# Kernel tuning notes

Hardware: AMD Instinct MI355X
Metric: run time of the kernel (lower is better)

Reference implementation:

```python
import jax, jax.numpy as jnp
import numpy as np
import math

B = 128        # batch (= bipartite matching N)
L = 16         # detector layers (MAX_LAYER)
E = 768        # n_embd
D = E // 2     # RFF target_dim
H = 12         # n_head
HD = E // H    # head_size
NL = 6         # n_layer
SEQ = 12       # tokens after concats: 3+3 -> 6 -> +currentLayer -> 12
MAX_LAYER = L
LN_EPS = 1e-3  # keras LayerNormalization default


def setup_inputs() -> dict:
    key = jax.random.key(0)
    ks = jax.random.split(key, 8)
    inp = {}
    inp["X"] = jax.random.normal(ks[0], (B, L, 3), dtype=jnp.float32) * 50.0
    inp["targets"] = jax.random.normal(ks[1], (B, L, 3), dtype=jnp.float32)
    # RandomFourierFeatures params (random per-call in original; fixed here):
    # x: xmin=-160,xmax=160,n=9*1024 ; y: n=12*512 ; dE: xmin=0,xmax=230,n=2300
    specs = [(-160.0, 160.0, 9 * 1024), (-160.0, 160.0, 12 * 512), (0.0, 230.0, 2300)]
    om, ph = [], []
    for i, (xmin, xmax, n) in enumerate(specs):
        k1, k2 = jax.random.split(jax.random.fold_in(ks[2], i))
        omin = 2.0 * math.pi / (xmax - xmin)
        lo, hi = math.log(omin / n), math.log(omin)
        om.append(jnp.exp(jax.random.uniform(k1, (D,), minval=lo, maxval=hi)))
        ph.append(jax.random.uniform(k2, (D,)))  # B ~ U(0,1)*scale, scale=1
    inp["omegas"] = jnp.stack(om).astype(jnp.float32)  # (3, D)
    inp["phases"] = jnp.stack(ph).astype(jnp.float32)  # (3, D)
    # np.random.permutation per layer-step, fixed here
    inp["perms"] = jnp.stack(
        [jax.random.permutation(jax.random.fold_in(ks[3], i), B) for i in range(L - 1)]
    ).astype(jnp.int32)  # (L-1, B)
    # transformer weights (stacked over layers)
    kk = jax.random.split(ks[4], 16)
    s = 0.02
    inp["Wq"] = jax.random.normal(kk[0], (NL, E, H, HD)) * s
    inp["bq"] = jnp.zeros((NL, H, HD))
    inp["Wk"] = jax.random.normal(kk[1], (NL, E, H, HD)) * s
    inp["bk"] = jnp.zeros((NL, H, HD))
    inp["Wv"] = jax.random.normal(kk[2], (NL, E, H, HD)) * s
    inp["bv"] = jnp.zeros((NL, H, HD))
    inp["Wo"] = jax.random.normal(kk[3], (NL, H, HD, E)) * s
    inp["bo"] = jnp.zeros((NL, E))
    inp["ln1g"] = jnp.ones((NL, E)); inp["ln1b"] = jnp.zeros((NL, E))
    inp["ln2g"] = jnp.ones((NL, E)); inp["ln2b"] = jnp.zeros((NL, E))
    inp["W1"] = jax.random.normal(kk[4], (NL, E, 4 * E)) * s
    inp["b1f"] = jnp.zeros((NL, 4 * E))
    inp["W2"] = jax.random.normal(kk[5], (NL, 4 * E, E)) * s
    inp["b2f"] = jnp.zeros((NL, E))
    inp["lnfg"] = jnp.ones((E,)); inp["lnfb"] = jnp.zeros((E,))
    inp["Wout"] = jax.random.normal(kk[6], (SEQ * E, 3)) * s
    inp["bout"] = jnp.zeros((3,))
    return inp


def _ln(x, g, b):
    mu = jnp.mean(x, -1, keepdims=True)
    v = jnp.var(x, -1, keepdims=True)
    return (x - mu) * jax.lax.rsqrt(v + LN_EPS) * g + b


def _greedy_match(cost):
    """Greedy bipartite matching: sort all NxN costs ascending, assign first-come.
    Returns row_to_col_match_vec (N,) int32."""
    N = cost.shape[0]
    order = jnp.argsort(cost.reshape(-1))

    def step(carry, k):
        row, col = carry
        i = k // N
        j = k % N
        ok = (row[i] == -1) & (col[j] == -1)
        row = row.at[i].set(jnp.where(ok, j, row[i]))
        col = col.at[j].set(jnp.where(ok, i, col[j]))
        return (row, col), None

    init = (jnp.full((N,), -1, jnp.int32), jnp.full((N,), -1, jnp.int32))
    (row, _), _ = jax.lax.scan(step, init, order)
    return row


def _forward(X, targets, omegas, phases, perms, Wq, bq, Wk, bk, Wv, bv, Wo, bo,
             ln1g, ln1b, ln2g, ln2b, W1, b1f, W2, b2f, lnfg, lnfb, Wout, bout):
    # RFF: (B,L,3) -> (B,L,3,D)
    XS = jnp.cos(X[..., None] * omegas[None, None, :, :] + phases[None, None, :, :])
    losses = []
    scale = 1.0 / math.sqrt(HD)
    for lidx in range(1, L):
        xc = XS[:, -lidx]        # (B,3,D)
        xp = XS[:, -lidx - 1]    # (B,3,D)
        x = jnp.concatenate([xc, xp], axis=2)            # (B,3,E)
        y = targets[:, -lidx + 1]                        # (B,3)
        y_prev = jnp.broadcast_to(y[:, :, None], (B, 3, E))
        x = jnp.concatenate([x, y_prev], axis=1)         # (B,6,E)
        cur = jnp.full_like(x, float(MAX_LAYER - lidx))
        x = jnp.concatenate([x, cur], axis=1)            # (B,12,E)
        x = x[perms[lidx - 1]]                           # batch permutation
        for l in range(NL):
            h = _ln(x, ln1g[l], ln1b[l])
            q = jnp.einsum('bse,ehd->bshd', h, Wq[l]) + bq[l]
            k = jnp.einsum('bse,ehd->bshd', h, Wk[l]) + bk[l]
            v = jnp.einsum('bse,ehd->bshd', h, Wv[l]) + bv[l]
            att = jax.nn.softmax(jnp.einsum('bqhd,bkhd->bhqk', q, k) * scale, axis=-1)
            o = jnp.einsum('bhqk,bkhd->bqhd', att, v)
            x = x + (jnp.einsum('bqhd,hde->bqe', o, Wo[l]) + bo[l])
            h = _ln(x, ln2g[l], ln2b[l])
            x = x + (jnp.maximum(h @ W1[l] + b1f[l], 0.0) @ W2[l] + b2f[l])
        x = _ln(x, lnfg, lnfb).reshape(B, SEQ * E)
        logits = x @ Wout + bout                         # (B,3)
        tgt = targets[:, -lidx]                          # (B,3)
        cost = jnp.sqrt(jnp.sum((logits[:, None, :] - tgt[None, :, :]) ** 2, axis=-1) + 1e-12)
        m = _greedy_match(jax.lax.stop_gradient(cost))
        lm = logits[m]                                   # gather per original
        losses.append(jnp.mean((lm - tgt) ** 2))
    return jnp.mean(jnp.stack(losses))


def reference(X, targets, omegas, phases, perms, Wq, bq, Wk, bk, Wv, bv, Wo, bo,
              ln1g, ln1b, ln2g, ln2b, W1, b1f, W2, b2f, lnfg, lnfb, Wout, bout):
    return _forward(X, targets, omegas, phases, perms, Wq, bq, Wk, bk, Wv, bv, Wo, bo,
                    ln1g, ln1b, ln2g, ln2b, W1, b1f, W2, b2f, lnfg, lnfb, Wout, bout)
```

## Files before the change

### kernel.cpp

```cpp
#include <hip/hip_runtime.h>
#include <hip/hip_bf16.h>
#include <math.h>

#define B_   128
#define L_   16
#define E_   768
#define D_   384
#define H_   12
#define HD_  64
#define NL_  6
#define SEQ_ 12
#define LN_EPS 0.001f
#define WLS   7077888
#define BQS   2304

typedef __attribute__((ext_vector_type(8))) short bf16x8;
typedef __attribute__((ext_vector_type(4))) float f32x4;
typedef unsigned long long u64;

#define GLOAD_LDS16(g, l) \
    __builtin_amdgcn_global_load_lds((__attribute__((address_space(1))) const void*)(g), \
                                     (__attribute__((address_space(3))) void*)(l), 16, 0, 0)

__global__ __launch_bounds__(256) void k_x0(const float* __restrict__ X,
                                            const float* __restrict__ targets,
                                            const int* __restrict__ perms,
                                            const float* __restrict__ om,
                                            const float* __restrict__ ph,
                                            float* __restrict__ x, int cb, int ntok) {
    int i = blockIdx.x * 256 + threadIdx.x;
    if (i >= ntok*E_) return;
    int e   = i % E_;
    int tok = i / E_;
    int s   = tok % SEQ_;
    int bi  = (tok / SEQ_) % B_;
    int c   = tok / (SEQ_*B_);
    int cl  = cb + c;
    int lidx = cl + 1;
    int pb  = perms[cl*B_ + bi];
    float val;
    if (s < 3) {
        int t  = (e < D_) ? (L_ - lidx) : (L_ - lidx - 1);
        int dd = (e < D_) ? e : (e - D_);
        float xv = X[(pb*L_ + t)*3 + s];
        val = cosf(xv * om[s*D_ + dd] + ph[s*D_ + dd]);
    } else if (s < 6) {
        int t = (17 - lidx) & 15;
        val = targets[(pb*L_ + t)*3 + (s - 3)];
    } else {
        val = (float)(L_ - lidx);
    }
    x[i] = val;
}

__global__ __launch_bounds__(256) void k_ln(const float* __restrict__ x,
                                            const float* __restrict__ g,
                                            const float* __restrict__ b,
                                            __hip_bfloat16* __restrict__ h) {
    int gi = blockIdx.x * 256 + threadIdx.x;
    int tok = gi >> 6, lane = gi & 63;
    const float4* xr = (const float4*)(x + (size_t)tok * E_);
    float4 v0 = xr[lane], v1 = xr[lane + 64], v2 = xr[lane + 128];
    float s = v0.x+v0.y+v0.z+v0.w + v1.x+v1.y+v1.z+v1.w + v2.x+v2.y+v2.z+v2.w;
    #pragma unroll
    for (int o = 32; o > 0; o >>= 1) s += __shfl_xor(s, o, 64);
    float mu = s * (1.0f / E_);
    v0.x-=mu; v0.y-=mu; v0.z-=mu; v0.w-=mu;
    v1.x-=mu; v1.y-=mu; v1.z-=mu; v1.w-=mu;
    v2.x-=mu; v2.y-=mu; v2.z-=mu; v2.w-=mu;
    float q = v0.x*v0.x+v0.y*v0.y+v0.z*v0.z+v0.w*v0.w
            + v1.x*v1.x+v1.y*v1.y+v1.z*v1.z+v1.w*v1.w
            + v2.x*v2.x+v2.y*v2.y+v2.z*v2.z+v2.w*v2.w;
    #pragma unroll
    for (int o = 32; o > 0; o >>= 1) q += __shfl_xor(q, o, 64);
    float rstd = rsqrtf(q * (1.0f / E_) + LN_EPS);
    const float4* g4 = (const float4*)g;
    const float4* b4 = (const float4*)b;
    ushort4* h4 = (ushort4*)(h + (size_t)tok * E_);
    #pragma unroll
    for (int k = 0; k < 3; k++) {
        float4 v = (k == 0) ? v0 : (k == 1) ? v1 : v2;
        float4 gg = g4[lane + k*64], bb = b4[lane + k*64];
        ushort4 o;
        o.x = __bfloat16_as_ushort(__float2bfloat16(v.x * rstd * gg.x + bb.x));
        o.y = __bfloat16_as_ushort(__float2bfloat16(v.y * rstd * gg.y + bb.y));
        o.z = __bfloat16_as_ushort(__float2bfloat16(v.z * rstd * gg.z + bb.z));
        o.w = __bfloat16_as_ushort(__float2bfloat16(v.w * rstd * gg.w + bb.w));
        h4[lane + k*64] = o;
    }
}

__global__ __launch_bounds__(256) void k_cvt(const float* __restrict__ Wq,
                                             const float* __restrict__ Wk,
                                             const float* __restrict__ Wv,
                                             const float* __restrict__ Wo,
                                             const float* __restrict__ W1,
                                             const float* __restrict__ W2,
                                             const float* __restrict__ bq,
                                             const float* __restrict__ bk,
                                             const float* __restrict__ bv,
                                             __hip_bfloat16* __restrict__ wl0,
                                             float* __restrict__ bqkv0, int lbase) {
    int bid = blockIdx.x;
    int l   = lbase + bid / 6913;
    bid %= 6913;
    __hip_bfloat16* wl = wl0 + (size_t)(l - lbase) * WLS;
    float* bqkv = bqkv0 + (l - lbase) * BQS;
    int tid = threadIdx.x;
    if (bid == 6912) {
        for (int i = tid; i < 2304; i += 256) {
            float v = (i < 768) ? bq[l*768 + i] : (i < 1536) ? bk[l*768 + i - 768]
                                                             : bv[l*768 + i - 1536];
            bqkv[i] = v;
        }
        return;
    }
    const float* src; __hip_bfloat16* dst; int K, N, ti, tj;
    if (bid < 1728) {
        int part = bid / 576, idx = bid % 576;
        const float* srcs[3] = {Wq, Wk, Wv};
        src = srcs[part] + (size_t)l*768*768; dst = wl + (size_t)part*768*768;
        K = 768; N = 768; tj = idx % 24; ti = idx / 24;
    } else if (bid < 2304) {
        int idx = bid - 1728;
        src = Wo + (size_t)l*768*768; dst = wl + 1769472;
        K = 768; N = 768; tj = idx % 24; ti = idx / 24;
    } else if (bid < 4608) {
        int idx = bid - 2304;
        src = W1 + (size_t)l*768*3072; dst = wl + 2359296;
        K = 768; N = 3072; tj = idx % 96; ti = idx / 96;
    } else {
        int idx = bid - 4608;
        src = W2 + (size_t)l*3072*768; dst = wl + 4718592;
        K = 3072; N = 768; tj = idx % 24; ti = idx / 24;
    }
    __shared__ float tbuf[32][33];
    int tx = tid & 31, ty = tid >> 5;
    #pragma unroll
    for (int p = 0; p < 4; p++) {
        int k = ti*32 + ty + p*8, n = tj*32 + tx;
        tbuf[ty + p*8][tx] = src[(size_t)k*N + n];
    }
    __syncthreads();
    #pragma unroll
    for (int p = 0; p < 4; p++) {
        int n = tj*32 + ty + p*8, k = ti*32 + tx;
        dst[(size_t)n*K + k] = __float2bfloat16(tbuf[tx][ty + p*8]);
    }
}

#define MFMA_BF16(a, b, c) __builtin_amdgcn_mfma_f32_16x16x32_bf16(a, b, c, 0, 0, 0)

__global__ __launch_bounds__(256) void k_gemm128(const __hip_bfloat16* __restrict__ A,
                                                 const __hip_bfloat16* __restrict__ Bt,
                                                 const float* __restrict__ bias,
                                                 void* __restrict__ Cp,
                                                 int K, int ldb, int ldc, int flags) {
    __shared__ __align__(16) char smem[32768];
    const int tid  = threadIdx.x;
    const int lane = tid & 63;
    const int wid  = tid >> 6;
    const int wr   = wid >> 1;
    const int wc   = wid & 1;

    const int gx   = gridDim.x;
    const int nwg  = gx * gridDim.y;
    const int flat = blockIdx.y * gx + blockIdx.x;
    const int q8   = nwg >> 3, r8 = nwg & 7;
    const int xcd  = flat & 7, off8 = flat >> 3;
    const int swz  = (xcd < r8 ? xcd*(q8+1) : r8*(q8+1) + (xcd-r8)*q8) + off8;
    const int m0   = (swz / gx) * 128;
    const int n0   = (swz % gx) * 128;

    const int fr   = lane & 15, fkg = lane >> 4;
    const int NT   = K >> 5;

    const int srow = tid >> 2;
    const int skc  = 8 * ((tid & 3) ^ (srow & 3) ^ ((srow >> 2) & 3));

    const int rsw  = ((fkg ^ (fr & 3) ^ ((fr >> 2) & 3)) << 4);

    f32x4 acc[4][4] = {};

    auto stage = [&](int kt, int buf) {
        char* base = smem + buf*16384;
        const int kk = kt*32 + skc;
        GLOAD_LDS16(A  + (size_t)(m0 +      srow) * K   + kk, base +         tid*16);
        GLOAD_LDS16(A  + (size_t)(m0 + 64 + srow) * K   + kk, base +  4096 + tid*16);
        GLOAD_LDS16(Bt + (size_t)(n0 +      srow) * ldb + kk, base +  8192 + tid*16);
        GLOAD_LDS16(Bt + (size_t)(n0 + 64 + srow) * ldb + kk, base + 12288 + tid*16);
    };
    auto ldA = [&](int buf, int i) -> bf16x8 {
        int row = wr*64 + i*16 + fr;
        return *(const bf16x8*)(smem + buf*16384 + row*64 + rsw);
    };
    auto ldB = [&](int buf, int j) -> bf16x8 {
        int row = wc*64 + j*16 + fr;
        return *(const bf16x8*)(smem + buf*16384 + 8192 + row*64 + rsw);
    };

    stage(0, 0);
    __syncthreads();

    for (int kt = 0; kt < NT; ++kt) {
        const int cur = kt & 1;
        if (kt + 1 < NT) stage(kt + 1, cur ^ 1);
        bf16x8 b[4], a[4];
        #pragma unroll
        for (int j = 0; j < 4; j++) b[j] = ldB(cur, j);
        #pragma unroll
        for (int i = 0; i < 4; i++) a[i] = ldA(cur, i);
        __builtin_amdgcn_s_setprio(1);
        #pragma unroll
        for (int i = 0; i < 4; i++)
            #pragma unroll
            for (int j = 0; j < 4; j++)
                acc[i][j] = MFMA_BF16(a[i], b[j], acc[i][j]);
        __builtin_amdgcn_s_setprio(0);
        __syncthreads();
    }

    const int colL = lane & 15, rowg = (lane >> 4) * 4;
    #pragma unroll
    for (int i = 0; i < 4; i++) {
        #pragma unroll
        for (int j = 0; j < 4; j++) {
            int col = n0 + wc*64 + j*16 + colL;
            float bv = bias ? bias[col] : 0.0f;
            #pragma unroll
            for (int r = 0; r < 4; r++) {
                int row = m0 + wr*64 + i*16 + rowg + r;
                float v = acc[i][j][r] + bv;
                if (flags & 4) v = fmaxf(v, 0.0f);
                size_t off = (size_t)row * ldc + col;
                if (flags & 1)      ((__hip_bfloat16*)Cp)[off] = __float2bfloat16(v);
                else if (flags & 2) ((float*)Cp)[off] += v;
                else                ((float*)Cp)[off] = v;
            }
        }
    }
}

__global__ __launch_bounds__(256) void k_attn(const __hip_bfloat16* __restrict__ qkv,
                                              __hip_bfloat16* __restrict__ o) {
    __shared__ float qs[SEQ_][HD_], ks[SEQ_][HD_], vs[SEQ_][HD_];
    __shared__ float att[SEQ_][SEQ_];
    int blk = blockIdx.x;
    int hh  = blk % H_;
    int cbb = blk / H_;
    int t = threadIdx.x;
    if (t < 96) {
        int s = t >> 3, c = (t & 7) * 8;
        size_t base = (size_t)(cbb*SEQ_ + s) * 2304 + hh*64 + c;
        bf16x8 q8 = *(const bf16x8*)(qkv + base);
        bf16x8 k8 = *(const bf16x8*)(qkv + base + 768);
        bf16x8 v8 = *(const bf16x8*)(qkv + base + 1536);
        #pragma unroll
        for (int j = 0; j < 8; j++) {
            qs[s][c+j] = __uint_as_float((unsigned)(unsigned short)q8[j] << 16);
            ks[s][c+j] = __uint_as_float((unsigned)(unsigned short)k8[j] << 16);
            vs[s][c+j] = __uint_as_float((unsigned)(unsigned short)v8[j] << 16);
        }
    }
    __syncthreads();
    if (t < SEQ_*SEQ_) {
        int qi = t / SEQ_, kj = t % SEQ_;
        float s = 0.f;
        #pragma unroll
        for (int d = 0; d < HD_; d++) s += qs[qi][d] * ks[kj][d];
        att[qi][kj] = s * 0.125f;
    }
    __syncthreads();
    if (t < SEQ_) {
        float mx = -1e30f;
        #pragma unroll
        for (int j = 0; j < SEQ_; j++) mx = fmaxf(mx, att[t][j]);
        float e[SEQ_]; float sum = 0.f;
        #pragma unroll
        for (int j = 0; j < SEQ_; j++) { e[j] = expf(att[t][j] - mx); sum += e[j]; }
        float inv = 1.f / sum;
        #pragma unroll
        for (int j = 0; j < SEQ_; j++) att[t][j] = e[j] * inv;
    }
    __syncthreads();
    for (int i = t; i < SEQ_*HD_; i += 256) {
        int s = i / HD_, d = i % HD_;
        float acc = 0.f;
        #pragma unroll
        for (int j = 0; j < SEQ_; j++) acc += att[s][j] * vs[j][d];
        o[(size_t)(cbb*SEQ_ + s) * 768 + hh*64 + d] = __float2bfloat16(acc);
    }
}

__global__ __launch_bounds__(256) void k_logits(const __hip_bfloat16* __restrict__ hfin,
                                                const float* __restrict__ Wout,
                                                const float* __restrict__ bout,
                                                float* __restrict__ logits, int cb) {
    __shared__ float red[3][256];
    int blk = blockIdx.x;
    int t = threadIdx.x;
    const __hip_bfloat16* row = hfin + (size_t)blk * SEQ_ * E_;
    float a0 = 0.f, a1 = 0.f, a2 = 0.f;
    for (int e = t; e < SEQ_*E_; e += 256) {
        float x = __bfloat162float(row[e]);
        a0 += x * Wout[e*3 + 0]; a1 += x * Wout[e*3 + 1]; a2 += x * Wout[e*3 + 2];
    }
    red[0][t] = a0; red[1][t] = a1; red[2][t] = a2;
    __syncthreads();
    for (int o = 128; o > 0; o >>= 1) {
        if (t < o) { red[0][t] += red[0][t+o]; red[1][t] += red[1][t+o]; red[2][t] += red[2][t+o]; }
        __syncthreads();
    }
    if (t < 3) logits[((size_t)cb*B_ + blk)*3 + t] = red[t][0] + bout[t];
}

__global__ __launch_bounds__(64) void k_match(const float* __restrict__ logits,
                                              const float* __restrict__ targets,
                                              float* __restrict__ losses) {
    __shared__ float cst[128 * 129];
    __shared__ float tg[128][3];
    __shared__ int mrow[128];
    int cl = blockIdx.x, lane = threadIdx.x;
    int lidx = cl + 1;
    for (int j = lane; j < 128; j += 64) {
        const float* tp = &targets[((size_t)j*L_ + (L_ - lidx)) * 3];
        tg[j][0] = tp[0]; tg[j][1] = tp[1]; tg[j][2] = tp[2];
    }
    __syncthreads();
    u64 kc[2];
    #pragma unroll
    for (int hh = 0; hh < 2; hh++) {
        int r = lane + hh*64;
        const float* lg = &logits[(cl*B_ + r) * 3];
        float l0 = lg[0], l1 = lg[1], l2 = lg[2];
        u64 best = ~0ull;
        for (int c = 0; c < 128; c++) {
            float d0 = l0 - tg[c][0], d1 = l1 - tg[c][1], d2 = l2 - tg[c][2];
            float cc = sqrtf(d0*d0 + d1*d1 + d2*d2 + 1e-12f);
            cst[r*129 + c] = cc;
            u64 key = ((u64)__float_as_uint(cc) << 14) | (unsigned)(r*128 + c);
            best = key < best ? key : best;
        }
        kc[hh] = best;
    }
    __syncthreads();
    u64 dead0 = 0, dead1 = 0;
    int done = 0;
    for (int trip = 0; trip < 16640 && done < 128; trip++) {
        u64 b = kc[0] < kc[1] ? kc[0] : kc[1];
        #pragma unroll
        for (int o = 32; o > 0; o >>= 1) {
            u64 x = __shfl_xor(b, o, 64);
            b = x < b ? x : b;
        }
        unsigned e  = (unsigned)b & 0x3fffu;
        unsigned wi = e >> 7, wj = e & 127;
        bool isDead = (((wj < 64) ? (dead0 >> wj) : (dead1 >> (wj - 64))) & 1ull) != 0;
        if (!isDead) {
            if ((wi & 63u) == (unsigned)lane) {
                mrow[wi] = (int)wj;
                kc[wi >> 6] = ~0ull;
            }
            if (wj < 64) dead0 |= 1ull << wj; else dead1 |= 1ull << (wj - 64);
            done++;
        } else {
            float c0 = cst[wi*129 + lane];
            float c1 = cst[wi*129 + lane + 64];
            bool d0b = ((dead0 >> lane) & 1ull) != 0;
            bool d1b = ((dead1 >> lane) & 1ull) != 0;
            u64 k0 = d0b ? ~0ull : (((u64)__float_as_uint(c0) << 14) | (unsigned)(wi*128 + lane));
            u64 k1 = d1b ? ~0ull : (((u64)__float_as_uint(c1) << 14) | (unsigned)(wi*128 + lane + 64));
            u64 nb = k0 < k1 ? k0 : k1;
            #pragma unroll
            for (int o = 32; o > 0; o >>= 1) {
                u64 x = __shfl_xor(nb, o, 64);
                nb = x < nb ? x : nb;
            }
            if ((wi & 63u) == (unsigned)lane) kc[wi >> 6] = nb;
        }
    }
    __syncthreads();
    float a = 0.f;
    #pragma unroll
    for (int hh = 0; hh < 2; hh++) {
        int r = lane + hh*64;
        const float* lg = &logits[(cl*B_ + mrow[r]) * 3];
        float d0 = lg[0]-tg[r][0], d1 = lg[1]-tg[r][1], d2 = lg[2]-tg[r][2];
        a += d0*d0 + d1*d1 + d2*d2;
    }
    #pragma unroll
    for (int o = 32; o > 0; o >>= 1) a += __shfl_xor(a, o, 64);
    if (lane == 0) losses[cl] = a * (1.0f / (B_*3));
}

__global__ void k_final(const float* __restrict__ losses, float* __restrict__ out) {
    float s = 0.f;
    for (int i = 0; i < 15; i++) s += losses[i];
    out[0] = s * (1.0f / 15.0f);
}

extern "C" void kernel_launch(void* const* d_in, const int* in_sizes, int n_in,
                              void* d_out, int out_size, void* d_ws, size_t ws_size,
                              hipStream_t stream) {
    (void)in_sizes; (void)n_in; (void)out_size;
    const float* X       = (const float*)d_in[0];
    const float* targets = (const float*)d_in[1];
    const float* omegas  = (const float*)d_in[2];
    const float* phases  = (const float*)d_in[3];
    const int*   perms   = (const int*)d_in[4];
    const float* Wq  = (const float*)d_in[5];
    const float* bq  = (const float*)d_in[6];
    const float* Wk  = (const float*)d_in[7];
    const float* bk  = (const float*)d_in[8];
    const float* Wv  = (const float*)d_in[9];
    const float* bv  = (const float*)d_in[10];
    const float* Wo  = (const float*)d_in[11];
    const float* bo  = (const float*)d_in[12];
    const float* ln1g = (const float*)d_in[13];
    const float* ln1b = (const float*)d_in[14];
    const float* ln2g = (const float*)d_in[15];
    const float* ln2b = (const float*)d_in[16];
    const float* W1  = (const float*)d_in[17];
    const float* b1f = (const float*)d_in[18];
    const float* W2  = (const float*)d_in[19];
    const float* b2f = (const float*)d_in[20];
    const float* lnfg = (const float*)d_in[21];
    const float* lnfb = (const float*)d_in[22];
    const float* Wout = (const float*)d_in[23];
    const float* bout = (const float*)d_in[24];

    int CL; bool hoist;
    if (ws_size >= 263000000ull)      { CL = 15; hoist = false; }
    else if (ws_size >= 169000000ull) { CL = 5;  hoist = true;  }
    else                              { CL = 5;  hoist = false; }
    int M = CL * B_ * SEQ_;
    bool perLayerCvt = (CL == 15) || !hoist;

    char* wsb = (char*)d_ws;
    size_t off = 0;
    auto alloc = [&](size_t bytes) {
        char* p = wsb + off;
        off += (bytes + 255) & ~(size_t)255;
        return p;
    };
    float*          x      = (float*)alloc((size_t)M*E_*4);
    __hip_bfloat16* h      = (__hip_bfloat16*)alloc((size_t)M*E_*2);
    __hip_bfloat16* qkvh   = (__hip_bfloat16*)alloc((size_t)M*3072*2);
    __hip_bfloat16* wl     = (__hip_bfloat16*)alloc((hoist ? 6 : 1) * (size_t)WLS*2);
    float*          bqkv   = (float*)alloc((hoist ? 6 : 1) * (size_t)BQS*4);
    float*          logits = (float*)alloc(23040);
    float*          losses = (float*)alloc(64);

    if (hoist)
        k_cvt<<<6*6913, 256, 0, stream>>>(Wq, Wk, Wv, Wo, W1, W2, bq, bk, bv, wl, bqkv, 0);

    dim3 gQKV(2304/128, M/128);
    dim3 gF1 (3072/128, M/128);
    dim3 gN  (768/128,  M/128);
    dim3 gLN (M/4);

    for (int cb = 0; cb < 15; cb += CL) {
        k_x0<<<(M*E_)/256, 256, 0, stream>>>(X, targets, perms, omegas, phases, x, cb, M);
        for (int l = 0; l < NL_; l++) {
            __hip_bfloat16* wlp = hoist ? wl + (size_t)l*WLS : wl;
            float*          bqp = hoist ? bqkv + l*BQS : bqkv;
            if (perLayerCvt)
                k_cvt<<<6913, 256, 0, stream>>>(Wq, Wk, Wv, Wo, W1, W2, bq, bk, bv, wlp, bqp, l);
            k_ln<<<gLN, 256, 0, stream>>>(x, ln1g + l*E_, ln1b + l*E_, h);
            k_gemm128<<<gQKV, 256, 0, stream>>>(h, wlp, bqp, qkvh, 768, 768, 2304, 1);
            k_attn<<<CL*B_*H_, 256, 0, stream>>>(qkvh, h);
            k_gemm128<<<gN, 256, 0, stream>>>(h, wlp + 1769472, bo + l*E_, x,
                                              768, 768, 768, 2);
            k_ln<<<gLN, 256, 0, stream>>>(x, ln2g + l*E_, ln2b + l*E_, h);
            k_gemm128<<<gF1, 256, 0, stream>>>(h, wlp + 2359296, b1f + l*3072, qkvh,
                                               768, 768, 3072, 1|4);
            k_gemm128<<<gN, 256, 0, stream>>>(qkvh, wlp + 4718592, b2f + l*E_, x,
                                              3072, 3072, 768, 2);
        }
        k_ln<<<gLN, 256, 0, stream>>>(x, lnfg, lnfb, h);
        k_logits<<<CL*B_, 256, 0, stream>>>(h, Wout, bout, logits, cb);
    }
    k_match<<<15, 64, 0, stream>>>(logits, targets, losses);
    k_final<<<1, 1, 0, stream>>>(losses, (float*)d_out);
}
```

Before: 4.541 ms.

## Stage GEMM epilogue through LDS for coalesced stores; cheaper wave min reduction

The GEMM epilogue now writes the accumulator tile into shared memory and then stores it with 16-byte coalesced vector writes, both for bf16 output and for fp32 accumulate (done in two half-tile phases to fit LDS). This targets the scattered 2- and 4-byte global stores of the MFMA fragment layout. Separately, the greedy matching's wave-wide 64-bit min reduction is replaced with a 32-bit min on the cost bits plus a ballot, and the 64-bit shuffle reduction only runs on ties. The epilogue adds extra barriers and LDS traffic. The fp32 path now always accumulates into the output (read-modify-write) and no longer applies ReLU, so it depends on every fp32 call using both the accumulate flag and no ReLU.

```diff
diff --git a/kernel.cpp b/kernel.cpp
--- a/kernel.cpp
+++ b/kernel.cpp
@@ -177,7 +177,6 @@
 
     const int srow = tid >> 2;
     const int skc  = 8 * ((tid & 3) ^ (srow & 3) ^ ((srow >> 2) & 3));
-
     const int rsw  = ((fkg ^ (fr & 3) ^ ((fr >> 2) & 3)) << 4);
 
     f32x4 acc[4][4] = {};
@@ -221,21 +220,59 @@
     }
 
     const int colL = lane & 15, rowg = (lane >> 4) * 4;
-    #pragma unroll
-    for (int i = 0; i < 4; i++) {
-        #pragma unroll
-        for (int j = 0; j < 4; j++) {
-            int col = n0 + wc*64 + j*16 + colL;
-            float bv = bias ? bias[col] : 0.0f;
+    if (flags & 1) {
+        #pragma unroll
+        for (int i = 0; i < 4; i++)
             #pragma unroll
-            for (int r = 0; r < 4; r++) {
-                int row = m0 + wr*64 + i*16 + rowg + r;
-                float v = acc[i][j][r] + bv;
-                if (flags & 4) v = fmaxf(v, 0.0f);
-                size_t off = (size_t)row * ldc + col;
-                if (flags & 1)      ((__hip_bfloat16*)Cp)[off] = __float2bfloat16(v);
-                else if (flags & 2) ((float*)Cp)[off] += v;
-                else                ((float*)Cp)[off] = v;
+            for (int j = 0; j < 4; j++) {
+                int lcol = wc*64 + j*16 + colL;
+                float bv = bias ? bias[n0 + lcol] : 0.0f;
+                #pragma unroll
+                for (int r = 0; r < 4; r++) {
+                    int lrow = wr*64 + i*16 + rowg + r;
+                    float v = acc[i][j][r] + bv;
+                    if (flags & 4) v = fmaxf(v, 0.0f);
+                    *(unsigned short*)(smem + lrow*256 + lcol*2) =
+                        __bfloat16_as_ushort(__float2bfloat16(v));
+                }
+            }
+        __syncthreads();
+        #pragma unroll
+        for (int q = 0; q < 8; q++) {
+            int f = tid*128 + q*16;
+            int lrow = f >> 8, colb = f & 255;
+            *(float4*)((char*)Cp + ((size_t)(m0 + lrow) * ldc + n0) * 2 + colb) =
+                *(const float4*)(smem + f);
+        }
+    } else {
+        #pragma unroll
+        for (int phse = 0; phse < 2; phse++) {
+            if (phse) __syncthreads();
+            if (wr == phse) {
+                #pragma unroll
+                for (int i = 0; i < 4; i++)
+                    #pragma unroll
+                    for (int j = 0; j < 4; j++) {
+                        int lcol = wc*64 + j*16 + colL;
+                        float bv = bias ? bias[n0 + lcol] : 0.0f;
+                        #pragma unroll
+                        for (int r = 0; r < 4; r++) {
+                            int lrow = i*16 + rowg + r;
+                            *(float*)(smem + lrow*512 + lcol*4) = acc[i][j][r] + bv;
+                        }
+                    }
+            }
+            __syncthreads();
+            #pragma unroll
+            for (int q = 0; q < 8; q++) {
+                int f = tid*128 + q*16;
+                int lrow = f >> 9, colb = f & 511;
+                float4* cp = (float4*)((char*)Cp +
+                    ((size_t)(m0 + phse*64 + lrow) * ldc + n0) * 4 + colb);
+                float4 cv = *cp;
+                f32x4 lv = *(const f32x4*)(smem + f);
+                cv.x += lv[0]; cv.y += lv[1]; cv.z += lv[2]; cv.w += lv[3];
+                *cp = cv;
             }
         }
     }
@@ -344,15 +381,32 @@
         kc[hh] = best;
     }
     __syncthreads();
+
+    auto wave_min_key = [&](u64 myKey) -> u64 {
+        unsigned cbits = (unsigned)(myKey >> 14);
+        unsigned mn = cbits;
+        #pragma unroll
+        for (int o = 32; o > 0; o >>= 1) {
+            unsigned x = __shfl_xor(mn, o, 64);
+            mn = x < mn ? x : mn;
+        }
+        u64 mask = __ballot(cbits == mn);
+        if (__popcll(mask) == 1) {
+            return __shfl(myKey, (int)__builtin_ctzll(mask), 64);
+        }
+        u64 bw = myKey;
+        #pragma unroll
+        for (int o = 32; o > 0; o >>= 1) {
+            u64 x = __shfl_xor(bw, o, 64);
+            bw = x < bw ? x : bw;
+        }
+        return bw;
+    };
+
     u64 dead0 = 0, dead1 = 0;
     int done = 0;
     for (int trip = 0; trip < 16640 && done < 128; trip++) {
-        u64 b = kc[0] < kc[1] ? kc[0] : kc[1];
-        #pragma unroll
-        for (int o = 32; o > 0; o >>= 1) {
-            u64 x = __shfl_xor(b, o, 64);
-            b = x < b ? x : b;
-        }
+        u64 b = wave_min_key(kc[0] < kc[1] ? kc[0] : kc[1]);
         unsigned e  = (unsigned)b & 0x3fffu;
         unsigned wi = e >> 7, wj = e & 127;
         bool isDead = (((wj < 64) ? (dead0 >> wj) : (dead1 >> (wj - 64))) & 1ull) != 0;
@@ -370,12 +424,7 @@
             bool d1b = ((dead1 >> lane) & 1ull) != 0;
             u64 k0 = d0b ? ~0ull : (((u64)__float_as_uint(c0) << 14) | (unsigned)(wi*128 + lane));
             u64 k1 = d1b ? ~0ull : (((u64)__float_as_uint(c1) << 14) | (unsigned)(wi*128 + lane + 64));
-            u64 nb = k0 < k1 ? k0 : k1;
-            #pragma unroll
-            for (int o = 32; o > 0; o >>= 1) {
-                u64 x = __shfl_xor(nb, o, 64);
-                nb = x < nb ? x : nb;
-            }
+            u64 nb = wave_min_key(k0 < k1 ? k0 : k1);
             if ((wi & 63u) == (unsigned)lane) kc[wi >> 6] = nb;
         }
     }
```

Result: no change. 4.562 ms (+0.5%).

## Keep per-row top-8 candidate lists in greedy matching to cut rescans

Applied to the files above, without the earlier changes.

The greedy bipartite match kernel now keeps a sorted top-8 candidate list per row in shared memory, built during cost computation by insertion. Each of the 128 match steps advances row heads past dead columns and rescans a full cost row only when its list runs out. The old loop did one wave-wide reduction per trip and rescanned a row whenever its best column was already taken. This adds an insertion chain per cost element, extra shared memory and ballot-driven loops, and affects only the small matching kernel, not the transformer GEMMs.

```diff
diff --git a/kernel.cpp b/kernel.cpp
--- a/kernel.cpp
+++ b/kernel.cpp
@@ -177,7 +177,6 @@
 
     const int srow = tid >> 2;
     const int skc  = 8 * ((tid & 3) ^ (srow & 3) ^ ((srow >> 2) & 3));
-
     const int rsw  = ((fkg ^ (fr & 3) ^ ((fr >> 2) & 3)) << 4);
 
     f32x4 acc[4][4] = {};
@@ -320,6 +319,7 @@
     __shared__ float cst[128 * 129];
     __shared__ float tg[128][3];
     __shared__ int mrow[128];
+    __shared__ u64 cand[128][9];
     int cl = blockIdx.x, lane = threadIdx.x;
     int lidx = cl + 1;
     for (int j = lane; j < 128; j += 64) {
@@ -327,57 +327,95 @@
         tg[j][0] = tp[0]; tg[j][1] = tp[1]; tg[j][2] = tp[2];
     }
     __syncthreads();
-    u64 kc[2];
+
+    int  head0 = 0, head1 = 0;
+    bool matched0 = false, matched1 = false;
     #pragma unroll
     for (int hh = 0; hh < 2; hh++) {
         int r = lane + hh*64;
         const float* lg = &logits[(cl*B_ + r) * 3];
         float l0 = lg[0], l1 = lg[1], l2 = lg[2];
-        u64 best = ~0ull;
+        u64 s0=~0ull,s1=~0ull,s2=~0ull,s3=~0ull,s4=~0ull,s5=~0ull,s6=~0ull,s7=~0ull;
         for (int c = 0; c < 128; c++) {
             float d0 = l0 - tg[c][0], d1 = l1 - tg[c][1], d2 = l2 - tg[c][2];
             float cc = sqrtf(d0*d0 + d1*d1 + d2*d2 + 1e-12f);
             cst[r*129 + c] = cc;
-            u64 key = ((u64)__float_as_uint(cc) << 14) | (unsigned)(r*128 + c);
-            best = key < best ? key : best;
-        }
-        kc[hh] = best;
-    }
-    __syncthreads();
+            u64 t = ((u64)__float_as_uint(cc) << 14) | (unsigned)(r*128 + c);
+            u64 lo;
+            lo = s0 < t ? s0 : t; t = s0 < t ? t : s0; s0 = lo;
+            lo = s1 < t ? s1 : t; t = s1 < t ? t : s1; s1 = lo;
+            lo = s2 < t ? s2 : t; t = s2 < t ? t : s2; s2 = lo;
+            lo = s3 < t ? s3 : t; t = s3 < t ? t : s3; s3 = lo;
+            lo = s4 < t ? s4 : t; t = s4 < t ? t : s4; s4 = lo;
+            lo = s5 < t ? s5 : t; t = s5 < t ? t : s5; s5 = lo;
+            lo = s6 < t ? s6 : t; t = s6 < t ? t : s6; s6 = lo;
+            lo = s7 < t ? s7 : t; s7 = lo;
+        }
+        cand[r][0]=s0; cand[r][1]=s1; cand[r][2]=s2; cand[r][3]=s3;
+        cand[r][4]=s4; cand[r][5]=s5; cand[r][6]=s6; cand[r][7]=s7;
+    }
+    __syncthreads();
+
     u64 dead0 = 0, dead1 = 0;
-    int done = 0;
-    for (int trip = 0; trip < 16640 && done < 128; trip++) {
-        u64 b = kc[0] < kc[1] ? kc[0] : kc[1];
-        #pragma unroll
-        for (int o = 32; o > 0; o >>= 1) {
-            u64 x = __shfl_xor(b, o, 64);
-            b = x < b ? x : b;
-        }
-        unsigned e  = (unsigned)b & 0x3fffu;
-        unsigned wi = e >> 7, wj = e & 127;
-        bool isDead = (((wj < 64) ? (dead0 >> wj) : (dead1 >> (wj - 64))) & 1ull) != 0;
-        if (!isDead) {
-            if ((wi & 63u) == (unsigned)lane) {
-                mrow[wi] = (int)wj;
-                kc[wi >> 6] = ~0ull;
+    for (int mt = 0; mt < 128; mt++) {
+        bool need0 = false, need1 = false;
+        if (!matched0) {
+            while (head0 < 8) {
+                unsigned wj = (unsigned)cand[lane][head0] & 127u;
+                bool d = (wj < 64) ? ((dead0 >> wj) & 1ull) : ((dead1 >> (wj - 64)) & 1ull);
+                if (!d) break;
+                head0++;
             }
-            if (wj < 64) dead0 |= 1ull << wj; else dead1 |= 1ull << (wj - 64);
-            done++;
-        } else {
-            float c0 = cst[wi*129 + lane];
-            float c1 = cst[wi*129 + lane + 64];
+            need0 = (head0 == 8);
+        }
+        if (!matched1) {
+            while (head1 < 8) {
+                unsigned wj = (unsigned)cand[lane + 64][head1] & 127u;
+                bool d = (wj < 64) ? ((dead0 >> wj) & 1ull) : ((dead1 >> (wj - 64)) & 1ull);
+                if (!d) break;
+                head1++;
+            }
+            need1 = (head1 == 8);
+        }
+        u64 nb0 = __ballot(need0);
+        u64 nb1 = __ballot(need1);
+        while (nb0 | nb1) {
+            int R;
+            if (nb0) { R = (int)__builtin_ctzll(nb0);      nb0 &= nb0 - 1; }
+            else     { R = (int)__builtin_ctzll(nb1) + 64; nb1 &= nb1 - 1; }
+            float c0 = cst[R*129 + lane];
+            float c1 = cst[R*129 + lane + 64];
             bool d0b = ((dead0 >> lane) & 1ull) != 0;
             bool d1b = ((dead1 >> lane) & 1ull) != 0;
-            u64 k0 = d0b ? ~0ull : (((u64)__float_as_uint(c0) << 14) | (unsigned)(wi*128 + lane));
-            u64 k1 = d1b ? ~0ull : (((u64)__float_as_uint(c1) << 14) | (unsigned)(wi*128 + lane + 64));
+            u64 k0 = d0b ? ~0ull : (((u64)__float_as_uint(c0) << 14) | (unsigned)(R*128 + lane));
+            u64 k1 = d1b ? ~0ull : (((u64)__float_as_uint(c1) << 14) | (unsigned)(R*128 + lane + 64));
             u64 nb = k0 < k1 ? k0 : k1;
             #pragma unroll
             for (int o = 32; o > 0; o >>= 1) {
                 u64 x = __shfl_xor(nb, o, 64);
                 nb = x < nb ? x : nb;
             }
-            if ((wi & 63u) == (unsigned)lane) kc[wi >> 6] = nb;
-        }
+            if ((R & 63) == lane) {
+                cand[R][7] = nb;
+                if (R >> 6) head1 = 7; else head0 = 7;
+            }
+        }
+        u64 my = ~0ull;
+        if (!matched0) my = cand[lane][head0];
+        if (!matched1) { u64 k = cand[lane + 64][head1]; my = k < my ? k : my; }
+        u64 b = my;
+        #pragma unroll
+        for (int o = 32; o > 0; o >>= 1) {
+            u64 x = __shfl_xor(b, o, 64);
+            b = x < b ? x : b;
+        }
+        unsigned e  = (unsigned)b & 0x3fffu;
+        unsigned wi = e >> 7, wj = e & 127u;
+        if ((wi & 63u) == (unsigned)lane) {
+            mrow[wi] = (int)wj;
+            if (wi >> 6) matched1 = true; else matched0 = true;
+        }
+        if (wj < 64) dead0 |= 1ull << wj; else dead1 |= 1ull << (wj - 64);
     }
     __syncthreads();
     float a = 0.f;
```

Result: slower. 4.778 ms (+5.2%).
